# Kernel optimization log

Hardware: AMD Instinct MI355X
Metric: run time of the kernel (lower is better)

The kernel has to match this reference:

```python
import jax, jax.numpy as jnp
import numpy as np

V, D, B, L = 433, 120, 4096, 16  # vocab, d_model, batch, seq_len
H4 = 4 * D
LN_EPS = 1e-5


def setup_inputs() -> dict:
    key = jax.random.key(0)
    ks = jax.random.split(key, 12)
    s = 1.0 / np.sqrt(D)  # PyTorch LSTM init range
    u = lambda k, shape: jax.random.uniform(k, shape, jnp.float32, -s, s)
    return {
        "x": jax.random.randint(ks[0], (B, L), 0, V, dtype=jnp.int32),
        "embed": jax.random.normal(ks[1], (V, D), jnp.float32) * 0.02,
        "Wih0": u(ks[2], (H4, D)), "Whh0": u(ks[3], (H4, D)),
        "bih0": u(ks[4], (H4,)), "bhh0": u(ks[5], (H4,)),
        "Wih1": u(ks[6], (H4, D)), "Whh1": u(ks[7], (H4, D)),
        "bih1": u(ks[8], (H4,)), "bhh1": u(ks[9], (H4,)),
        "gamma": jnp.ones((D,), jnp.float32),
        "beta": jnp.zeros((D,), jnp.float32),
    }


def _lstm_layer(x, Wih, Whh, bih, bhh):
    """One LSTM layer, batch_first input [B,L,D] -> [B,L,H]. PyTorch gate order i,f,g,o."""
    b, _, _ = x.shape
    h_dim = Whh.shape[1]
    # Precompute input contribution for all timesteps in one big GEMM.
    xg = jnp.einsum('bld,gd->blg', x, Wih) + bih + bhh  # [B,L,4H]

    def step(carry, g_t):
        h, c = carry
        gates = g_t + h @ Whh.T  # [B,4H]
        i, f, g, o = jnp.split(gates, 4, axis=-1)
        c = jax.nn.sigmoid(f) * c + jax.nn.sigmoid(i) * jnp.tanh(g)
        h = jax.nn.sigmoid(o) * jnp.tanh(c)
        return (h, c), h

    init = (jnp.zeros((b, h_dim), x.dtype), jnp.zeros((b, h_dim), x.dtype))
    _, hs = jax.lax.scan(step, init, jnp.swapaxes(xg, 0, 1))  # [L,B,H]
    return jnp.swapaxes(hs, 0, 1)


def _layernorm(h, gamma, beta):
    mu = jnp.mean(h, axis=-1, keepdims=True)
    var = jnp.mean(jnp.square(h - mu), axis=-1, keepdims=True)
    return (h - mu) / jnp.sqrt(var + LN_EPS) * gamma + beta


def reference(x, embed, Wih0, Whh0, bih0, bhh0, Wih1, Whh1, bih1, bhh1, gamma, beta):
    h = embed[x]                               # [B,L,D] token embedding
    h = _lstm_layer(h, Wih0, Whh0, bih0, bhh0)  # layer 0
    h = _lstm_layer(h, Wih1, Whh1, bih1, bhh1)  # layer 1
    out = _layernorm(h, gamma, beta)
    logits = jnp.einsum('bld,vd->blv', out, embed)  # tied-embedding head (no bias)
    return logits
```

## Files before the change

kernel.cpp:

```cpp
#include <hip/hip_runtime.h>


#define VSZ 433
#define DIM 120
#define BSZ 4096
#define SEQ 16
#define H4  480
#define MTOT (BSZ*SEQ)
#define KP  128
#define NPAD 448
#define NT_HEAD (NPAD/16)
#define TB  16
#define GP  484
#define HP  136

typedef unsigned int   u32;
typedef unsigned short u16;
typedef __attribute__((ext_vector_type(8))) short    v8bf;
typedef __attribute__((ext_vector_type(8))) _Float16 v8h;
typedef __attribute__((ext_vector_type(4))) float    v4f;

__device__ __forceinline__ float bf2f(u16 u){ union{u32 i;float f;}z; z.i=((u32)u)<<16; return z.f; }
__device__ __forceinline__ u16 f2bf(float f){
  union{float f;u32 u;}z; z.f=f;
  u32 u = z.u + 0x7fffu + ((z.u>>16)&1u);
  return (u16)(u>>16);
}
__device__ __forceinline__ u32 packh2(float a, float b){
  union{_Float16 h[2]; u32 u;} z;
  z.h[0] = (_Float16)a; z.h[1] = (_Float16)b;
  return z.u;
}

#define EW_OFF   0u
#define B1S_OFF  831488u
#define EMBP_OFF 833408u
#define HB0_OFF  948096u

__global__ __launch_bounds__(512) void k_ew(const float* __restrict__ embed,
                                            const float* __restrict__ Wih0,
                                            const float* __restrict__ bih0,
                                            const float* __restrict__ bhh0,
                                            float* __restrict__ EW)
{
  __shared__ float e[DIM];
  const int v = blockIdx.x, tid = threadIdx.x;
  if (tid < DIM) e[tid] = embed[v*DIM + tid];
  __syncthreads();
  if (tid < H4) {
    float acc = bih0[tid] + bhh0[tid];
    #pragma unroll
    for (int k0 = 0; k0 < DIM; k0 += 4) {
      float4 w = *(const float4*)(Wih0 + tid*DIM + k0);
      acc = fmaf(e[k0+0], w.x, acc);
      acc = fmaf(e[k0+1], w.y, acc);
      acc = fmaf(e[k0+2], w.z, acc);
      acc = fmaf(e[k0+3], w.w, acc);
    }
    EW[v*H4 + tid] = acc;
  }
}

__global__ __launch_bounds__(256) void k_prep2(const float* __restrict__ embed,
                                               const float* __restrict__ bih1,
                                               const float* __restrict__ bhh1,
                                               u16* __restrict__ embP,
                                               float* __restrict__ b1s)
{
  const int idx = blockIdx.x*256 + threadIdx.x;
  if (idx < NPAD*KP) {
    int n = idx >> 7, k = idx & 127;
    embP[idx] = (n < VSZ && k < DIM) ? f2bf(embed[n*DIM + k]) : (u16)0;
  } else if (idx < NPAD*KP + H4) {
    int g = idx - NPAD*KP;
    b1s[g] = bih1[g] + bhh1[g];
  }
}

__global__ __launch_bounds__(512) void k_rec0(const float* __restrict__ Whh,
                                              const float* __restrict__ EW,
                                              const int* __restrict__ x,
                                              _Float16* __restrict__ hb0)
{
  __shared__ float gLs[TB][GP];
  __shared__ __align__(16) _Float16 hLh[TB][HP];
  __shared__ int xL[TB*SEQ];

  const int tid  = threadIdx.x;
  const int wave = tid >> 6, lane = tid & 63;
  const int cl   = lane & 15, quad = lane >> 4;
  const int b0   = blockIdx.x * TB;

  for (int i = tid; i < TB*SEQ; i += 512) xL[i] = x[b0*SEQ + i];
  for (int i = tid; i < TB*HP; i += 512) (&hLh[0][0])[i] = (_Float16)0.f;
  __syncthreads();

  v8h Bf[4][4];
  #pragma unroll
  for (int i = 0; i < 4; ++i) {
    const int nt = wave*4 + i;
    const bool vld = (nt < 30);
    const int n = vld ? nt*16 + cl : 0;
    #pragma unroll
    for (int kt = 0; kt < 4; ++kt) {
      const int k0 = kt*32 + quad*8;
      v8h f = {0,0,0,0,0,0,0,0};
      if (vld && k0 < DIM) {
        float4 q0 = *(const float4*)(Whh + n*DIM + k0);
        float4 q1 = *(const float4*)(Whh + n*DIM + k0 + 4);
        f[0]=(_Float16)q0.x; f[1]=(_Float16)q0.y; f[2]=(_Float16)q0.z; f[3]=(_Float16)q0.w;
        f[4]=(_Float16)q1.x; f[5]=(_Float16)q1.y; f[6]=(_Float16)q1.z; f[7]=(_Float16)q1.w;
      }
      Bf[i][kt] = f;
    }
  }

  float srcv[4][4];
  auto load_src = [&](int t) {
    #pragma unroll
    for (int i = 0; i < 4; ++i) {
      const int nt = wave*4 + i;
      if (nt < 30) {
        const int n = nt*16 + cl;
        #pragma unroll
        for (int r = 0; r < 4; ++r)
          srcv[i][r] = EW[(size_t)xL[(quad*4 + r)*SEQ + t]*H4 + n];
      }
    }
  };
  load_src(0);

  const int prow = wave*2;
  const bool act = lane < 60;
  const int d0   = lane*2;
  float C[2][2] = {{0.f,0.f},{0.f,0.f}};

  for (int t = 0; t < SEQ; ++t) {
    __syncthreads();
    v8h Af[4];
    #pragma unroll
    for (int kt = 0; kt < 4; ++kt)
      Af[kt] = *(const v8h*)&hLh[cl][kt*32 + quad*8];
    v4f acc[4];
    #pragma unroll
    for (int i = 0; i < 4; ++i) {
      acc[i][0]=srcv[i][0]; acc[i][1]=srcv[i][1];
      acc[i][2]=srcv[i][2]; acc[i][3]=srcv[i][3];
    }
    #pragma unroll
    for (int i = 0; i < 4; ++i)
      if (wave*4 + i < 30) {
        #pragma unroll
        for (int kt = 0; kt < 4; ++kt)
          acc[i] = __builtin_amdgcn_mfma_f32_16x16x32_f16(Af[kt], Bf[i][kt], acc[i], 0, 0, 0);
      }
    if (t + 1 < SEQ) load_src(t + 1);
    #pragma unroll
    for (int i = 0; i < 4; ++i) {
      const int nt = wave*4 + i;
      if (nt < 30) {
        #pragma unroll
        for (int r = 0; r < 4; ++r)
          gLs[quad*4 + r][nt*16 + cl] = acc[i][r];
      }
    }
    __syncthreads();
    #pragma unroll
    for (int rr = 0; rr < 2; ++rr) {
      const int row = prow + rr;
      if (act) {
        const float2 gi = *(const float2*)&gLs[row][d0      ];
        const float2 gf = *(const float2*)&gLs[row][d0 + 120];
        const float2 gg = *(const float2*)&gLs[row][d0 + 240];
        const float2 go = *(const float2*)&gLs[row][d0 + 360];
        float h2[2];
        #pragma unroll
        for (int k = 0; k < 2; ++k) {
          const float vi = k ? gi.y : gi.x, vf = k ? gf.y : gf.x;
          const float vg = k ? gg.y : gg.x, vo = k ? go.y : go.x;
          const float si = 1.f / (1.f + __expf(-vi));
          const float sf = 1.f / (1.f + __expf(-vf));
          const float tg = 1.f - 2.f / (__expf(2.f*vg) + 1.f);
          const float so = 1.f / (1.f + __expf(-vo));
          const float c  = sf * C[rr][k] + si * tg;
          C[rr][k] = c;
          const float tc = 1.f - 2.f / (__expf(2.f*c) + 1.f);
          h2[k] = so * tc;
        }
        *(u32*)&hLh[row][d0] = packh2(h2[0], h2[1]);
        *(u32*)&hb0[((size_t)t*BSZ + b0 + row)*KP + d0] = packh2(h2[0], h2[1]);
      } else {
        *(u32*)&hb0[((size_t)t*BSZ + b0 + row)*KP + 120 + 2*(lane - 60)] = 0u;
      }
    }
  }
}

__global__ __launch_bounds__(512) void k_rec1(const float* __restrict__ Wih1,
                                              const float* __restrict__ Whh1,
                                              const float* __restrict__ b1s,
                                              const _Float16* __restrict__ hb0,
                                              const float* __restrict__ gamma,
                                              const float* __restrict__ beta,
                                              const u16* __restrict__ embP,
                                              float* __restrict__ out)
{
  __shared__ float gLs[TB][GP];
  __shared__ __align__(16) _Float16 hLh[TB][HP];
  __shared__ __align__(16) u16 hnL[TB][HP];
  __shared__ __align__(16) u16 embL[NPAD][HP];

  const int tid  = threadIdx.x;
  const int wave = tid >> 6, lane = tid & 63;
  const int cl   = lane & 15, quad = lane >> 4;
  const int b0   = blockIdx.x * TB;

  for (int i = tid; i < TB*HP; i += 512) (&hLh[0][0])[i] = (_Float16)0.f;
  for (int c = tid; c < NPAD*16; c += 512) {
    const int rw = c >> 4, c16 = c & 15;
    *(v8bf*)&embL[rw][c16*8] = *(const v8bf*)&embP[(size_t)rw*KP + c16*8];
  }

  v8h Bi[4][4], Bh[4][4];
  float bias[4];
  #pragma unroll
  for (int i = 0; i < 4; ++i) {
    const int nt = wave*4 + i;
    const bool vld = (nt < 30);
    const int n = vld ? nt*16 + cl : 0;
    bias[i] = vld ? b1s[n] : 0.f;
    #pragma unroll
    for (int kt = 0; kt < 4; ++kt) {
      const int k0 = kt*32 + quad*8;
      v8h fi = {0,0,0,0,0,0,0,0}, fh = {0,0,0,0,0,0,0,0};
      if (vld && k0 < DIM) {
        float4 q0 = *(const float4*)(Wih1 + n*DIM + k0);
        float4 q1 = *(const float4*)(Wih1 + n*DIM + k0 + 4);
        fi[0]=(_Float16)q0.x; fi[1]=(_Float16)q0.y; fi[2]=(_Float16)q0.z; fi[3]=(_Float16)q0.w;
        fi[4]=(_Float16)q1.x; fi[5]=(_Float16)q1.y; fi[6]=(_Float16)q1.z; fi[7]=(_Float16)q1.w;
        float4 p0 = *(const float4*)(Whh1 + n*DIM + k0);
        float4 p1 = *(const float4*)(Whh1 + n*DIM + k0 + 4);
        fh[0]=(_Float16)p0.x; fh[1]=(_Float16)p0.y; fh[2]=(_Float16)p0.z; fh[3]=(_Float16)p0.w;
        fh[4]=(_Float16)p1.x; fh[5]=(_Float16)p1.y; fh[6]=(_Float16)p1.z; fh[7]=(_Float16)p1.w;
      }
      Bi[i][kt] = fi;
      Bh[i][kt] = fh;
    }
  }

  const int prow = wave*2;
  const bool act = lane < 60;
  const int d0   = lane*2;
  float gmm[2] = {0.f, 0.f}, bta[2] = {0.f, 0.f};
  if (act) {
    gmm[0] = gamma[d0]; gmm[1] = gamma[d0+1];
    bta[0] = beta[d0];  bta[1] = beta[d0+1];
  }
  float C[2][2] = {{0.f,0.f},{0.f,0.f}};

  v8h A0n[4];
  #pragma unroll
  for (int kt = 0; kt < 4; ++kt)
    A0n[kt] = *(const v8h*)&hb0[((size_t)0*BSZ + b0 + cl)*KP + kt*32 + quad*8];
  __syncthreads();

  for (int t = 0; t < SEQ; ++t) {
    v8h A0c[4], A1[4];
    #pragma unroll
    for (int kt = 0; kt < 4; ++kt) A0c[kt] = A0n[kt];
    #pragma unroll
    for (int kt = 0; kt < 4; ++kt)
      A1[kt] = *(const v8h*)&hLh[cl][kt*32 + quad*8];
    if (t + 1 < SEQ) {
      #pragma unroll
      for (int kt = 0; kt < 4; ++kt)
        A0n[kt] = *(const v8h*)&hb0[((size_t)(t+1)*BSZ + b0 + cl)*KP + kt*32 + quad*8];
    }
    v4f acc[4];
    #pragma unroll
    for (int i = 0; i < 4; ++i)
      acc[i] = (v4f){bias[i], bias[i], bias[i], bias[i]};
    #pragma unroll
    for (int i = 0; i < 4; ++i)
      if (wave*4 + i < 30) {
        #pragma unroll
        for (int kt = 0; kt < 4; ++kt) {
          acc[i] = __builtin_amdgcn_mfma_f32_16x16x32_f16(A0c[kt], Bi[i][kt], acc[i], 0, 0, 0);
          acc[i] = __builtin_amdgcn_mfma_f32_16x16x32_f16(A1[kt],  Bh[i][kt], acc[i], 0, 0, 0);
        }
      }
    #pragma unroll
    for (int i = 0; i < 4; ++i) {
      const int nt = wave*4 + i;
      if (nt < 30) {
        #pragma unroll
        for (int r = 0; r < 4; ++r)
          gLs[quad*4 + r][nt*16 + cl] = acc[i][r];
      }
    }
    __syncthreads();
    float h2[2][2] = {{0.f,0.f},{0.f,0.f}};
    float s1[2] = {0.f, 0.f}, s2[2] = {0.f, 0.f};
    #pragma unroll
    for (int rr = 0; rr < 2; ++rr) {
      const int row = prow + rr;
      if (act) {
        const float2 gi = *(const float2*)&gLs[row][d0      ];
        const float2 gf = *(const float2*)&gLs[row][d0 + 120];
        const float2 gg = *(const float2*)&gLs[row][d0 + 240];
        const float2 go = *(const float2*)&gLs[row][d0 + 360];
        #pragma unroll
        for (int k = 0; k < 2; ++k) {
          const float vi = k ? gi.y : gi.x, vf = k ? gf.y : gf.x;
          const float vg = k ? gg.y : gg.x, vo = k ? go.y : go.x;
          const float si = 1.f / (1.f + __expf(-vi));
          const float sf = 1.f / (1.f + __expf(-vf));
          const float tg = 1.f - 2.f / (__expf(2.f*vg) + 1.f);
          const float so = 1.f / (1.f + __expf(-vo));
          const float c  = sf * C[rr][k] + si * tg;
          C[rr][k] = c;
          const float tc = 1.f - 2.f / (__expf(2.f*c) + 1.f);
          const float h  = so * tc;
          h2[rr][k] = h;
          s1[rr] += h;
          s2[rr] = fmaf(h, h, s2[rr]);
        }
        *(u32*)&hLh[row][d0] = packh2(h2[rr][0], h2[rr][1]);
      }
    }
    #pragma unroll
    for (int m = 32; m >= 1; m >>= 1) {
      s1[0] += __shfl_xor(s1[0], m);
      s2[0] += __shfl_xor(s2[0], m);
      s1[1] += __shfl_xor(s1[1], m);
      s2[1] += __shfl_xor(s2[1], m);
    }
    #pragma unroll
    for (int rr = 0; rr < 2; ++rr) {
      const int row = prow + rr;
      const float mu = s1[rr] * (1.f/DIM);
      const float var = s2[rr] * (1.f/DIM) - mu*mu;
      const float rs = rsqrtf(var + 1e-5f);
      if (act) {
        const float v0 = fmaf((h2[rr][0] - mu)*rs, gmm[0], bta[0]);
        const float v1 = fmaf((h2[rr][1] - mu)*rs, gmm[1], bta[1]);
        *(u32*)&hnL[row][d0] = (u32)f2bf(v0) | ((u32)f2bf(v1) << 16);
      } else {
        *(u32*)&hnL[row][120 + 2*(lane - 60)] = 0u;
      }
    }
    __syncthreads();

    {
      v8bf a[4];
      #pragma unroll
      for (int kt = 0; kt < 4; ++kt)
        a[kt] = *(const v8bf*)&hnL[cl][kt*32 + quad*8];
      #pragma unroll
      for (int j = 0; j < 4; ++j) {
        const int nt = wave + 8*j;
        if (nt < NT_HEAD) {
          const int n = nt*16 + cl;
          v8bf bfr[4];
          #pragma unroll
          for (int kt = 0; kt < 4; ++kt)
            bfr[kt] = *(const v8bf*)&embL[n][kt*32 + quad*8];
          v4f hacc = {0.f, 0.f, 0.f, 0.f};
          #pragma unroll
          for (int kt = 0; kt < 4; ++kt)
            hacc = __builtin_amdgcn_mfma_f32_16x16x32_bf16(a[kt], bfr[kt], hacc, 0, 0, 0);
          if (n < VSZ) {
            #pragma unroll
            for (int r = 0; r < 4; ++r)
              out[((size_t)(b0 + quad*4 + r)*SEQ + t)*VSZ + n] = hacc[r];
          }
        }
      }
    }
  }
}

extern "C" void kernel_launch(void* const* d_in, const int* in_sizes, int n_in,
                              void* d_out, int out_size, void* d_ws, size_t ws_size,
                              hipStream_t stream)
{
  (void)in_sizes; (void)n_in; (void)out_size; (void)ws_size;
  const int*   x     = (const int*)d_in[0];
  const float* embed = (const float*)d_in[1];
  const float* Wih0  = (const float*)d_in[2];
  const float* Whh0  = (const float*)d_in[3];
  const float* bih0  = (const float*)d_in[4];
  const float* bhh0  = (const float*)d_in[5];
  const float* Wih1  = (const float*)d_in[6];
  const float* Whh1  = (const float*)d_in[7];
  const float* bih1  = (const float*)d_in[8];
  const float* bhh1  = (const float*)d_in[9];
  const float* gamma = (const float*)d_in[10];
  const float* beta  = (const float*)d_in[11];

  char* ws = (char*)d_ws;
  float*     EW   = (float*)(ws + EW_OFF);
  float*     b1s  = (float*)(ws + B1S_OFF);
  u16*       embP = (u16*)(ws + EMBP_OFF);
  _Float16*  hb0  = (_Float16*)(ws + HB0_OFF);

  k_ew   <<<VSZ, 512, 0, stream>>>(embed, Wih0, bih0, bhh0, EW);
  k_prep2<<<226, 256, 0, stream>>>(embed, bih1, bhh1, embP, b1s);
  k_rec0 <<<BSZ/TB, 512, 0, stream>>>(Whh0, EW, x, hb0);
  k_rec1 <<<BSZ/TB, 512, 0, stream>>>(Wih1, Whh1, b1s, hb0, gamma, beta, embP, (float*)d_out);
}
```

Measured before the change: 258.3 us.

## Double threads per block in recurrent kernels and read head weights from MFMA-fragment layout

Both recurrent kernels now launch 1024 threads (16 waves) instead of 512, so each wave owns 2 gate tiles and one batch row instead of 4 tiles and two rows. This shortens the serial per-step work on each wave. The layer-1 kernel no longer stages the padded embedding in LDS. Instead it reads bf16 head weights straight from global memory in a fragment-ordered layout built by the prep kernel, and it uses the freed LDS to preload all 16 timesteps of layer-0 output. The trade-offs are more register and occupancy pressure, global or L2 traffic for the head weights on every step, and fewer resident blocks per CU.

```diff
diff --git a/kernel.cpp b/kernel.cpp
--- a/kernel.cpp
+++ b/kernel.cpp
@@ -6,10 +6,9 @@
 #define BSZ 4096
 #define SEQ 16
 #define H4  480
-#define MTOT (BSZ*SEQ)
 #define KP  128
 #define NPAD 448
-#define NT_HEAD (NPAD/16)
+#define NT_HEAD 28
 #define TB  16
 #define GP  484
 #define HP  136
@@ -20,7 +19,6 @@
 typedef __attribute__((ext_vector_type(8))) _Float16 v8h;
 typedef __attribute__((ext_vector_type(4))) float    v4f;
 
-__device__ __forceinline__ float bf2f(u16 u){ union{u32 i;float f;}z; z.i=((u32)u)<<16; return z.f; }
 __device__ __forceinline__ u16 f2bf(float f){
   union{float f;u32 u;}z; z.f=f;
   u32 u = z.u + 0x7fffu + ((z.u>>16)&1u);
@@ -34,7 +32,7 @@
 
 #define EW_OFF   0u
 #define B1S_OFF  831488u
-#define EMBP_OFF 833408u
+#define EMBF_OFF 833408u
 #define HB0_OFF  948096u
 
 __global__ __launch_bounds__(512) void k_ew(const float* __restrict__ embed,
@@ -64,23 +62,25 @@
 __global__ __launch_bounds__(256) void k_prep2(const float* __restrict__ embed,
                                                const float* __restrict__ bih1,
                                                const float* __restrict__ bhh1,
-                                               u16* __restrict__ embP,
+                                               u16* __restrict__ embF,
                                                float* __restrict__ b1s)
 {
   const int idx = blockIdx.x*256 + threadIdx.x;
   if (idx < NPAD*KP) {
     int n = idx >> 7, k = idx & 127;
-    embP[idx] = (n < VSZ && k < DIM) ? f2bf(embed[n*DIM + k]) : (u16)0;
+    int nt = n >> 4, cl = n & 15, kt = k >> 5, quad = (k >> 3) & 3, j = k & 7;
+    int fidx = ((((nt*4 + kt)*4 + quad)*16 + cl) << 3) + j;
+    embF[fidx] = (n < VSZ && k < DIM) ? f2bf(embed[n*DIM + k]) : (u16)0;
   } else if (idx < NPAD*KP + H4) {
     int g = idx - NPAD*KP;
     b1s[g] = bih1[g] + bhh1[g];
   }
 }
 
-__global__ __launch_bounds__(512) void k_rec0(const float* __restrict__ Whh,
-                                              const float* __restrict__ EW,
-                                              const int* __restrict__ x,
-                                              _Float16* __restrict__ hb0)
+__global__ __launch_bounds__(1024) void k_rec0(const float* __restrict__ Whh,
+                                               const float* __restrict__ EW,
+                                               const int* __restrict__ x,
+                                               _Float16* __restrict__ hb0)
 {
   __shared__ float gLs[TB][GP];
   __shared__ __align__(16) _Float16 hLh[TB][HP];
@@ -91,14 +91,15 @@
   const int cl   = lane & 15, quad = lane >> 4;
   const int b0   = blockIdx.x * TB;
 
-  for (int i = tid; i < TB*SEQ; i += 512) xL[i] = x[b0*SEQ + i];
-  for (int i = tid; i < TB*HP; i += 512) (&hLh[0][0])[i] = (_Float16)0.f;
+  for (int i = tid; i < TB*SEQ; i += 1024) xL[i] = x[b0*SEQ + i];
+  for (int i = tid; i < TB*HP; i += 1024) (&hLh[0][0])[i] = (_Float16)0.f;
   __syncthreads();
 
-  v8h Bf[4][4];
+  const int nt0 = wave*2, nt1 = wave*2 + 1;
+  v8h Bf[2][4];
   #pragma unroll
-  for (int i = 0; i < 4; ++i) {
-    const int nt = wave*4 + i;
+  for (int i = 0; i < 2; ++i) {
+    const int nt = wave*2 + i;
     const bool vld = (nt < 30);
     const int n = vld ? nt*16 + cl : 0;
     #pragma unroll
@@ -115,11 +116,11 @@
     }
   }
 
-  float srcv[4][4];
+  float srcv[2][4];
   auto load_src = [&](int t) {
     #pragma unroll
-    for (int i = 0; i < 4; ++i) {
-      const int nt = wave*4 + i;
+    for (int i = 0; i < 2; ++i) {
+      const int nt = wave*2 + i;
       if (nt < 30) {
         const int n = nt*16 + cl;
         #pragma unroll
@@ -130,34 +131,29 @@
   };
   load_src(0);
 
-  const int prow = wave*2;
+  const int row = wave;
   const bool act = lane < 60;
   const int d0   = lane*2;
-  float C[2][2] = {{0.f,0.f},{0.f,0.f}};
+  float C[2] = {0.f, 0.f};
 
   for (int t = 0; t < SEQ; ++t) {
     __syncthreads();
-    v8h Af[4];
-    #pragma unroll
-    for (int kt = 0; kt < 4; ++kt)
-      Af[kt] = *(const v8h*)&hLh[cl][kt*32 + quad*8];
-    v4f acc[4];
-    #pragma unroll
-    for (int i = 0; i < 4; ++i) {
+    v4f acc[2];
+    #pragma unroll
+    for (int i = 0; i < 2; ++i) {
       acc[i][0]=srcv[i][0]; acc[i][1]=srcv[i][1];
       acc[i][2]=srcv[i][2]; acc[i][3]=srcv[i][3];
     }
     #pragma unroll
-    for (int i = 0; i < 4; ++i)
-      if (wave*4 + i < 30) {
-        #pragma unroll
-        for (int kt = 0; kt < 4; ++kt)
-          acc[i] = __builtin_amdgcn_mfma_f32_16x16x32_f16(Af[kt], Bf[i][kt], acc[i], 0, 0, 0);
-      }
+    for (int kt = 0; kt < 4; ++kt) {
+      v8h A1 = *(const v8h*)&hLh[cl][kt*32 + quad*8];
+      if (nt0 < 30) acc[0] = __builtin_amdgcn_mfma_f32_16x16x32_f16(A1, Bf[0][kt], acc[0], 0, 0, 0);
+      if (nt1 < 30) acc[1] = __builtin_amdgcn_mfma_f32_16x16x32_f16(A1, Bf[1][kt], acc[1], 0, 0, 0);
+    }
     if (t + 1 < SEQ) load_src(t + 1);
     #pragma unroll
-    for (int i = 0; i < 4; ++i) {
-      const int nt = wave*4 + i;
+    for (int i = 0; i < 2; ++i) {
+      const int nt = wave*2 + i;
       if (nt < 30) {
         #pragma unroll
         for (int r = 0; r < 4; ++r)
@@ -165,67 +161,64 @@
       }
     }
     __syncthreads();
-    #pragma unroll
-    for (int rr = 0; rr < 2; ++rr) {
-      const int row = prow + rr;
-      if (act) {
-        const float2 gi = *(const float2*)&gLs[row][d0      ];
-        const float2 gf = *(const float2*)&gLs[row][d0 + 120];
-        const float2 gg = *(const float2*)&gLs[row][d0 + 240];
-        const float2 go = *(const float2*)&gLs[row][d0 + 360];
-        float h2[2];
-        #pragma unroll
-        for (int k = 0; k < 2; ++k) {
-          const float vi = k ? gi.y : gi.x, vf = k ? gf.y : gf.x;
-          const float vg = k ? gg.y : gg.x, vo = k ? go.y : go.x;
-          const float si = 1.f / (1.f + __expf(-vi));
-          const float sf = 1.f / (1.f + __expf(-vf));
-          const float tg = 1.f - 2.f / (__expf(2.f*vg) + 1.f);
-          const float so = 1.f / (1.f + __expf(-vo));
-          const float c  = sf * C[rr][k] + si * tg;
-          C[rr][k] = c;
-          const float tc = 1.f - 2.f / (__expf(2.f*c) + 1.f);
-          h2[k] = so * tc;
-        }
-        *(u32*)&hLh[row][d0] = packh2(h2[0], h2[1]);
-        *(u32*)&hb0[((size_t)t*BSZ + b0 + row)*KP + d0] = packh2(h2[0], h2[1]);
-      } else {
-        *(u32*)&hb0[((size_t)t*BSZ + b0 + row)*KP + 120 + 2*(lane - 60)] = 0u;
-      }
-    }
-  }
-}
-
-__global__ __launch_bounds__(512) void k_rec1(const float* __restrict__ Wih1,
-                                              const float* __restrict__ Whh1,
-                                              const float* __restrict__ b1s,
-                                              const _Float16* __restrict__ hb0,
-                                              const float* __restrict__ gamma,
-                                              const float* __restrict__ beta,
-                                              const u16* __restrict__ embP,
-                                              float* __restrict__ out)
+    if (act) {
+      const float2 gi = *(const float2*)&gLs[row][d0      ];
+      const float2 gf = *(const float2*)&gLs[row][d0 + 120];
+      const float2 gg = *(const float2*)&gLs[row][d0 + 240];
+      const float2 go = *(const float2*)&gLs[row][d0 + 360];
+      float h2[2];
+      #pragma unroll
+      for (int k = 0; k < 2; ++k) {
+        const float vi = k ? gi.y : gi.x, vf = k ? gf.y : gf.x;
+        const float vg = k ? gg.y : gg.x, vo = k ? go.y : go.x;
+        const float si = 1.f / (1.f + __expf(-vi));
+        const float sf = 1.f / (1.f + __expf(-vf));
+        const float tg = 1.f - 2.f / (__expf(2.f*vg) + 1.f);
+        const float so = 1.f / (1.f + __expf(-vo));
+        const float c  = sf * C[k] + si * tg;
+        C[k] = c;
+        const float tc = 1.f - 2.f / (__expf(2.f*c) + 1.f);
+        h2[k] = so * tc;
+      }
+      *(u32*)&hLh[row][d0] = packh2(h2[0], h2[1]);
+      *(u32*)&hb0[((size_t)t*BSZ + b0 + row)*KP + d0] = packh2(h2[0], h2[1]);
+    } else {
+      *(u32*)&hb0[((size_t)t*BSZ + b0 + row)*KP + 120 + 2*(lane - 60)] = 0u;
+    }
+  }
+}
+
+__global__ __launch_bounds__(1024) void k_rec1(const float* __restrict__ Wih1,
+                                               const float* __restrict__ Whh1,
+                                               const float* __restrict__ b1s,
+                                               const _Float16* __restrict__ hb0,
+                                               const float* __restrict__ gamma,
+                                               const float* __restrict__ beta,
+                                               const u16* __restrict__ embF,
+                                               float* __restrict__ out)
 {
   __shared__ float gLs[TB][GP];
   __shared__ __align__(16) _Float16 hLh[TB][HP];
   __shared__ __align__(16) u16 hnL[TB][HP];
-  __shared__ __align__(16) u16 embL[NPAD][HP];
+  __shared__ __align__(16) _Float16 hb0L[SEQ][TB][HP];
 
   const int tid  = threadIdx.x;
   const int wave = tid >> 6, lane = tid & 63;
   const int cl   = lane & 15, quad = lane >> 4;
   const int b0   = blockIdx.x * TB;
 
-  for (int i = tid; i < TB*HP; i += 512) (&hLh[0][0])[i] = (_Float16)0.f;
-  for (int c = tid; c < NPAD*16; c += 512) {
-    const int rw = c >> 4, c16 = c & 15;
-    *(v8bf*)&embL[rw][c16*8] = *(const v8bf*)&embP[(size_t)rw*KP + c16*8];
-  }
-
-  v8h Bi[4][4], Bh[4][4];
-  float bias[4];
+  for (int i = tid; i < TB*HP; i += 1024) (&hLh[0][0])[i] = (_Float16)0.f;
+  for (int c = tid; c < SEQ*TB*16; c += 1024) {
+    const int t = c >> 8, rem = c & 255, rw = rem >> 4, k8 = (rem & 15)*8;
+    *(v8h*)&hb0L[t][rw][k8] = *(const v8h*)&hb0[((size_t)t*BSZ + b0 + rw)*KP + k8];
+  }
+
+  const int nt0 = wave*2, nt1 = wave*2 + 1;
+  v8h Bi[2][4], Bh[2][4];
+  float bias[2];
   #pragma unroll
-  for (int i = 0; i < 4; ++i) {
-    const int nt = wave*4 + i;
+  for (int i = 0; i < 2; ++i) {
+    const int nt = wave*2 + i;
     const bool vld = (nt < 30);
     const int n = vld ? nt*16 + cl : 0;
     bias[i] = vld ? b1s[n] : 0.f;
@@ -248,7 +241,7 @@
     }
   }
 
-  const int prow = wave*2;
+  const int row = wave;
   const bool act = lane < 60;
   const int d0   = lane*2;
   float gmm[2] = {0.f, 0.f}, bta[2] = {0.f, 0.f};
@@ -256,42 +249,30 @@
     gmm[0] = gamma[d0]; gmm[1] = gamma[d0+1];
     bta[0] = beta[d0];  bta[1] = beta[d0+1];
   }
-  float C[2][2] = {{0.f,0.f},{0.f,0.f}};
-
-  v8h A0n[4];
-  #pragma unroll
-  for (int kt = 0; kt < 4; ++kt)
-    A0n[kt] = *(const v8h*)&hb0[((size_t)0*BSZ + b0 + cl)*KP + kt*32 + quad*8];
+  float C[2] = {0.f, 0.f};
   __syncthreads();
 
   for (int t = 0; t < SEQ; ++t) {
-    v8h A0c[4], A1[4];
-    #pragma unroll
-    for (int kt = 0; kt < 4; ++kt) A0c[kt] = A0n[kt];
-    #pragma unroll
-    for (int kt = 0; kt < 4; ++kt)
-      A1[kt] = *(const v8h*)&hLh[cl][kt*32 + quad*8];
-    if (t + 1 < SEQ) {
-      #pragma unroll
-      for (int kt = 0; kt < 4; ++kt)
-        A0n[kt] = *(const v8h*)&hb0[((size_t)(t+1)*BSZ + b0 + cl)*KP + kt*32 + quad*8];
-    }
-    v4f acc[4];
-    #pragma unroll
-    for (int i = 0; i < 4; ++i)
+    v4f acc[2];
+    #pragma unroll
+    for (int i = 0; i < 2; ++i)
       acc[i] = (v4f){bias[i], bias[i], bias[i], bias[i]};
     #pragma unroll
-    for (int i = 0; i < 4; ++i)
-      if (wave*4 + i < 30) {
-        #pragma unroll
-        for (int kt = 0; kt < 4; ++kt) {
-          acc[i] = __builtin_amdgcn_mfma_f32_16x16x32_f16(A0c[kt], Bi[i][kt], acc[i], 0, 0, 0);
-          acc[i] = __builtin_amdgcn_mfma_f32_16x16x32_f16(A1[kt],  Bh[i][kt], acc[i], 0, 0, 0);
-        }
-      }
-    #pragma unroll
-    for (int i = 0; i < 4; ++i) {
-      const int nt = wave*4 + i;
+    for (int kt = 0; kt < 4; ++kt) {
+      v8h A0 = *(const v8h*)&hb0L[t][cl][kt*32 + quad*8];
+      v8h A1 = *(const v8h*)&hLh[cl][kt*32 + quad*8];
+      if (nt0 < 30) {
+        acc[0] = __builtin_amdgcn_mfma_f32_16x16x32_f16(A0, Bi[0][kt], acc[0], 0, 0, 0);
+        acc[0] = __builtin_amdgcn_mfma_f32_16x16x32_f16(A1, Bh[0][kt], acc[0], 0, 0, 0);
+      }
+      if (nt1 < 30) {
+        acc[1] = __builtin_amdgcn_mfma_f32_16x16x32_f16(A0, Bi[1][kt], acc[1], 0, 0, 0);
+        acc[1] = __builtin_amdgcn_mfma_f32_16x16x32_f16(A1, Bh[1][kt], acc[1], 0, 0, 0);
+      }
+    }
+    #pragma unroll
+    for (int i = 0; i < 2; ++i) {
+      const int nt = wave*2 + i;
       if (nt < 30) {
         #pragma unroll
         for (int r = 0; r < 4; ++r)
@@ -299,51 +280,43 @@
       }
     }
     __syncthreads();
-    float h2[2][2] = {{0.f,0.f},{0.f,0.f}};
-    float s1[2] = {0.f, 0.f}, s2[2] = {0.f, 0.f};
-    #pragma unroll
-    for (int rr = 0; rr < 2; ++rr) {
-      const int row = prow + rr;
-      if (act) {
-        const float2 gi = *(const float2*)&gLs[row][d0      ];
-        const float2 gf = *(const float2*)&gLs[row][d0 + 120];
-        const float2 gg = *(const float2*)&gLs[row][d0 + 240];
-        const float2 go = *(const float2*)&gLs[row][d0 + 360];
-        #pragma unroll
-        for (int k = 0; k < 2; ++k) {
-          const float vi = k ? gi.y : gi.x, vf = k ? gf.y : gf.x;
-          const float vg = k ? gg.y : gg.x, vo = k ? go.y : go.x;
-          const float si = 1.f / (1.f + __expf(-vi));
-          const float sf = 1.f / (1.f + __expf(-vf));
-          const float tg = 1.f - 2.f / (__expf(2.f*vg) + 1.f);
-          const float so = 1.f / (1.f + __expf(-vo));
-          const float c  = sf * C[rr][k] + si * tg;
-          C[rr][k] = c;
-          const float tc = 1.f - 2.f / (__expf(2.f*c) + 1.f);
-          const float h  = so * tc;
-          h2[rr][k] = h;
-          s1[rr] += h;
-          s2[rr] = fmaf(h, h, s2[rr]);
-        }
-        *(u32*)&hLh[row][d0] = packh2(h2[rr][0], h2[rr][1]);
-      }
+    float h2[2] = {0.f, 0.f};
+    float s1 = 0.f, s2 = 0.f;
+    if (act) {
+      const float2 gi = *(const float2*)&gLs[row][d0      ];
+      const float2 gf = *(const float2*)&gLs[row][d0 + 120];
+      const float2 gg = *(const float2*)&gLs[row][d0 + 240];
+      const float2 go = *(const float2*)&gLs[row][d0 + 360];
+      #pragma unroll
+      for (int k = 0; k < 2; ++k) {
+        const float vi = k ? gi.y : gi.x, vf = k ? gf.y : gf.x;
+        const float vg = k ? gg.y : gg.x, vo = k ? go.y : go.x;
+        const float si = 1.f / (1.f + __expf(-vi));
+        const float sf = 1.f / (1.f + __expf(-vf));
+        const float tg = 1.f - 2.f / (__expf(2.f*vg) + 1.f);
+        const float so = 1.f / (1.f + __expf(-vo));
+        const float c  = sf * C[k] + si * tg;
+        C[k] = c;
+        const float tc = 1.f - 2.f / (__expf(2.f*c) + 1.f);
+        const float h  = so * tc;
+        h2[k] = h;
+        s1 += h;
+        s2 = fmaf(h, h, s2);
+      }
+      *(u32*)&hLh[row][d0] = packh2(h2[0], h2[1]);
     }
     #pragma unroll
     for (int m = 32; m >= 1; m >>= 1) {
-      s1[0] += __shfl_xor(s1[0], m);
-      s2[0] += __shfl_xor(s2[0], m);
-      s1[1] += __shfl_xor(s1[1], m);
-      s2[1] += __shfl_xor(s2[1], m);
-    }
-    #pragma unroll
-    for (int rr = 0; rr < 2; ++rr) {
-      const int row = prow + rr;
-      const float mu = s1[rr] * (1.f/DIM);
-      const float var = s2[rr] * (1.f/DIM) - mu*mu;
+      s1 += __shfl_xor(s1, m);
+      s2 += __shfl_xor(s2, m);
+    }
+    {
+      const float mu = s1 * (1.f/DIM);
+      const float var = s2 * (1.f/DIM) - mu*mu;
       const float rs = rsqrtf(var + 1e-5f);
       if (act) {
-        const float v0 = fmaf((h2[rr][0] - mu)*rs, gmm[0], bta[0]);
-        const float v1 = fmaf((h2[rr][1] - mu)*rs, gmm[1], bta[1]);
+        const float v0 = fmaf((h2[0] - mu)*rs, gmm[0], bta[0]);
+        const float v1 = fmaf((h2[1] - mu)*rs, gmm[1], bta[1]);
         *(u32*)&hnL[row][d0] = (u32)f2bf(v0) | ((u32)f2bf(v1) << 16);
       } else {
         *(u32*)&hnL[row][120 + 2*(lane - 60)] = 0u;
@@ -357,18 +330,18 @@
       for (int kt = 0; kt < 4; ++kt)
         a[kt] = *(const v8bf*)&hnL[cl][kt*32 + quad*8];
       #pragma unroll
-      for (int j = 0; j < 4; ++j) {
-        const int nt = wave + 8*j;
+      for (int j = 0; j < 2; ++j) {
+        const int nt = wave + 16*j;
         if (nt < NT_HEAD) {
-          const int n = nt*16 + cl;
           v8bf bfr[4];
           #pragma unroll
           for (int kt = 0; kt < 4; ++kt)
-            bfr[kt] = *(const v8bf*)&embL[n][kt*32 + quad*8];
+            bfr[kt] = *(const v8bf*)&embF[(((size_t)nt*4 + kt)*64 + lane)*8];
           v4f hacc = {0.f, 0.f, 0.f, 0.f};
           #pragma unroll
           for (int kt = 0; kt < 4; ++kt)
             hacc = __builtin_amdgcn_mfma_f32_16x16x32_bf16(a[kt], bfr[kt], hacc, 0, 0, 0);
+          const int n = nt*16 + cl;
           if (n < VSZ) {
             #pragma unroll
             for (int r = 0; r < 4; ++r)
@@ -401,11 +374,11 @@
   char* ws = (char*)d_ws;
   float*     EW   = (float*)(ws + EW_OFF);
   float*     b1s  = (float*)(ws + B1S_OFF);
-  u16*       embP = (u16*)(ws + EMBP_OFF);
+  u16*       embF = (u16*)(ws + EMBF_OFF);
   _Float16*  hb0  = (_Float16*)(ws + HB0_OFF);
 
   k_ew   <<<VSZ, 512, 0, stream>>>(embed, Wih0, bih0, bhh0, EW);
-  k_prep2<<<226, 256, 0, stream>>>(embed, bih1, bhh1, embP, b1s);
-  k_rec0 <<<BSZ/TB, 512, 0, stream>>>(Whh0, EW, x, hb0);
-  k_rec1 <<<BSZ/TB, 512, 0, stream>>>(Wih1, Whh1, b1s, hb0, gamma, beta, embP, (float*)d_out);
-}
+  k_prep2<<<226, 256, 0, stream>>>(embed, bih1, bhh1, embF, b1s);
+  k_rec0 <<<BSZ/TB, 1024, 0, stream>>>(Whh0, EW, x, hb0);
+  k_rec1 <<<BSZ/TB, 1024, 0, stream>>>(Wih1, Whh1, b1s, hb0, gamma, beta, embF, (float*)d_out);
+}
```

After: 287.8 us. 1.11x slower.

## Fuse both LSTM layers and head into one wavefront-pipelined recurrent kernel

Applied to the files above, without the earlier changes.

Merges the layer-0 and layer-1 recurrent kernels into a single kernel that runs layer 0 at step s, layer 1 at step s-1 and the tied-embedding head at step s-2 in the same loop iteration. This removes the global round trip of the layer-0 hidden states and one of the two per-step barrier chains. Wih1 and the embedding are pre-swizzled into MFMA fragment order in global memory and read directly, rather than kept in registers or staged in a large LDS copy. The cost is extra per-step global loads of the Wih1 and embedding fragments, plus higher register pressure from holding both layers' state.

```diff
diff --git a/kernel.cpp b/kernel.cpp
--- a/kernel.cpp
+++ b/kernel.cpp
@@ -6,10 +6,9 @@
 #define BSZ 4096
 #define SEQ 16
 #define H4  480
-#define MTOT (BSZ*SEQ)
 #define KP  128
 #define NPAD 448
-#define NT_HEAD (NPAD/16)
+#define NT_HEAD 28
 #define TB  16
 #define GP  484
 #define HP  136
@@ -20,7 +19,6 @@
 typedef __attribute__((ext_vector_type(8))) _Float16 v8h;
 typedef __attribute__((ext_vector_type(4))) float    v4f;
 
-__device__ __forceinline__ float bf2f(u16 u){ union{u32 i;float f;}z; z.i=((u32)u)<<16; return z.f; }
 __device__ __forceinline__ u16 f2bf(float f){
   union{float f;u32 u;}z; z.f=f;
   u32 u = z.u + 0x7fffu + ((z.u>>16)&1u);
@@ -34,8 +32,8 @@
 
 #define EW_OFF   0u
 #define B1S_OFF  831488u
-#define EMBP_OFF 833408u
-#define HB0_OFF  948096u
+#define EMBF_OFF 833408u
+#define W1F_OFF  948096u
 
 __global__ __launch_bounds__(512) void k_ew(const float* __restrict__ embed,
                                             const float* __restrict__ Wih0,
@@ -61,29 +59,48 @@
   }
 }
 
-__global__ __launch_bounds__(256) void k_prep2(const float* __restrict__ embed,
-                                               const float* __restrict__ bih1,
-                                               const float* __restrict__ bhh1,
-                                               u16* __restrict__ embP,
-                                               float* __restrict__ b1s)
+__global__ __launch_bounds__(256) void k_prep(const float* __restrict__ embed,
+                                              const float* __restrict__ bih1,
+                                              const float* __restrict__ bhh1,
+                                              const float* __restrict__ Wih1,
+                                              u16* __restrict__ embF,
+                                              float* __restrict__ b1s,
+                                              _Float16* __restrict__ w1F)
 {
   const int idx = blockIdx.x*256 + threadIdx.x;
   if (idx < NPAD*KP) {
     int n = idx >> 7, k = idx & 127;
-    embP[idx] = (n < VSZ && k < DIM) ? f2bf(embed[n*DIM + k]) : (u16)0;
+    int nt = n >> 4, cl = n & 15, kt = k >> 5, quad = (k >> 3) & 3, j = k & 7;
+    int fidx = ((((nt*4 + kt)*4 + quad)*16 + cl) << 3) + j;
+    embF[fidx] = (n < VSZ && k < DIM) ? f2bf(embed[n*DIM + k]) : (u16)0;
   } else if (idx < NPAD*KP + H4) {
     int g = idx - NPAD*KP;
     b1s[g] = bih1[g] + bhh1[g];
-  }
-}
-
-__global__ __launch_bounds__(512) void k_rec0(const float* __restrict__ Whh,
-                                              const float* __restrict__ EW,
-                                              const int* __restrict__ x,
-                                              _Float16* __restrict__ hb0)
+  } else if (idx < NPAD*KP + H4 + 30*4*512) {
+    int i0 = idx - (NPAD*KP + H4);
+    int f = i0 >> 9, r = i0 & 511, lane = r >> 3, j = r & 7;
+    int nt = f >> 2, kt = f & 3, cl = lane & 15, quad = lane >> 4;
+    int k = kt*32 + quad*8 + j, n = nt*16 + cl;
+    w1F[i0] = (k < DIM) ? (_Float16)Wih1[n*DIM + k] : (_Float16)0.f;
+  }
+}
+
+__global__ __launch_bounds__(512) void k_rec(const float* __restrict__ Whh0,
+                                             const float* __restrict__ EW,
+                                             const int* __restrict__ x,
+                                             const float* __restrict__ Whh1,
+                                             const float* __restrict__ b1s,
+                                             const float* __restrict__ gamma,
+                                             const float* __restrict__ beta,
+                                             const _Float16* __restrict__ w1F,
+                                             const u16* __restrict__ embF,
+                                             float* __restrict__ out)
 {
-  __shared__ float gLs[TB][GP];
-  __shared__ __align__(16) _Float16 hLh[TB][HP];
+  __shared__ float gLs0[TB][GP];
+  __shared__ float gLs1[TB][GP];
+  __shared__ __align__(16) _Float16 hLh0[TB][HP];
+  __shared__ __align__(16) _Float16 hLh1[TB][HP];
+  __shared__ __align__(16) u16 hnLD[2][TB][HP];
   __shared__ int xL[TB*SEQ];
 
   const int tid  = threadIdx.x;
@@ -92,26 +109,35 @@
   const int b0   = blockIdx.x * TB;
 
   for (int i = tid; i < TB*SEQ; i += 512) xL[i] = x[b0*SEQ + i];
-  for (int i = tid; i < TB*HP; i += 512) (&hLh[0][0])[i] = (_Float16)0.f;
-  __syncthreads();
-
-  v8h Bf[4][4];
+  for (int i = tid; i < TB*HP; i += 512) {
+    (&hLh0[0][0])[i] = (_Float16)0.f;
+    (&hLh1[0][0])[i] = (_Float16)0.f;
+  }
+
+  v8h Bf0[4][4], Bh1[4][4];
+  float bias[4];
   #pragma unroll
   for (int i = 0; i < 4; ++i) {
     const int nt = wave*4 + i;
     const bool vld = (nt < 30);
     const int n = vld ? nt*16 + cl : 0;
+    bias[i] = vld ? b1s[n] : 0.f;
     #pragma unroll
     for (int kt = 0; kt < 4; ++kt) {
       const int k0 = kt*32 + quad*8;
-      v8h f = {0,0,0,0,0,0,0,0};
+      v8h f0 = {0,0,0,0,0,0,0,0}, f1 = {0,0,0,0,0,0,0,0};
       if (vld && k0 < DIM) {
-        float4 q0 = *(const float4*)(Whh + n*DIM + k0);
-        float4 q1 = *(const float4*)(Whh + n*DIM + k0 + 4);
-        f[0]=(_Float16)q0.x; f[1]=(_Float16)q0.y; f[2]=(_Float16)q0.z; f[3]=(_Float16)q0.w;
-        f[4]=(_Float16)q1.x; f[5]=(_Float16)q1.y; f[6]=(_Float16)q1.z; f[7]=(_Float16)q1.w;
-      }
-      Bf[i][kt] = f;
+        float4 q0 = *(const float4*)(Whh0 + n*DIM + k0);
+        float4 q1 = *(const float4*)(Whh0 + n*DIM + k0 + 4);
+        f0[0]=(_Float16)q0.x; f0[1]=(_Float16)q0.y; f0[2]=(_Float16)q0.z; f0[3]=(_Float16)q0.w;
+        f0[4]=(_Float16)q1.x; f0[5]=(_Float16)q1.y; f0[6]=(_Float16)q1.z; f0[7]=(_Float16)q1.w;
+        float4 p0 = *(const float4*)(Whh1 + n*DIM + k0);
+        float4 p1 = *(const float4*)(Whh1 + n*DIM + k0 + 4);
+        f1[0]=(_Float16)p0.x; f1[1]=(_Float16)p0.y; f1[2]=(_Float16)p0.z; f1[3]=(_Float16)p0.w;
+        f1[4]=(_Float16)p1.x; f1[5]=(_Float16)p1.y; f1[6]=(_Float16)p1.z; f1[7]=(_Float16)p1.w;
+      }
+      Bf0[i][kt] = f0;
+      Bh1[i][kt] = f1;
     }
   }
 
@@ -133,247 +159,187 @@
   const int prow = wave*2;
   const bool act = lane < 60;
   const int d0   = lane*2;
-  float C[2][2] = {{0.f,0.f},{0.f,0.f}};
-
-  for (int t = 0; t < SEQ; ++t) {
-    __syncthreads();
-    v8h Af[4];
-    #pragma unroll
-    for (int kt = 0; kt < 4; ++kt)
-      Af[kt] = *(const v8h*)&hLh[cl][kt*32 + quad*8];
-    v4f acc[4];
-    #pragma unroll
-    for (int i = 0; i < 4; ++i) {
-      acc[i][0]=srcv[i][0]; acc[i][1]=srcv[i][1];
-      acc[i][2]=srcv[i][2]; acc[i][3]=srcv[i][3];
-    }
-    #pragma unroll
-    for (int i = 0; i < 4; ++i)
-      if (wave*4 + i < 30) {
-        #pragma unroll
-        for (int kt = 0; kt < 4; ++kt)
-          acc[i] = __builtin_amdgcn_mfma_f32_16x16x32_f16(Af[kt], Bf[i][kt], acc[i], 0, 0, 0);
-      }
-    if (t + 1 < SEQ) load_src(t + 1);
-    #pragma unroll
-    for (int i = 0; i < 4; ++i) {
-      const int nt = wave*4 + i;
-      if (nt < 30) {
-        #pragma unroll
-        for (int r = 0; r < 4; ++r)
-          gLs[quad*4 + r][nt*16 + cl] = acc[i][r];
-      }
-    }
-    __syncthreads();
-    #pragma unroll
-    for (int rr = 0; rr < 2; ++rr) {
-      const int row = prow + rr;
-      if (act) {
-        const float2 gi = *(const float2*)&gLs[row][d0      ];
-        const float2 gf = *(const float2*)&gLs[row][d0 + 120];
-        const float2 gg = *(const float2*)&gLs[row][d0 + 240];
-        const float2 go = *(const float2*)&gLs[row][d0 + 360];
-        float h2[2];
-        #pragma unroll
-        for (int k = 0; k < 2; ++k) {
-          const float vi = k ? gi.y : gi.x, vf = k ? gf.y : gf.x;
-          const float vg = k ? gg.y : gg.x, vo = k ? go.y : go.x;
-          const float si = 1.f / (1.f + __expf(-vi));
-          const float sf = 1.f / (1.f + __expf(-vf));
-          const float tg = 1.f - 2.f / (__expf(2.f*vg) + 1.f);
-          const float so = 1.f / (1.f + __expf(-vo));
-          const float c  = sf * C[rr][k] + si * tg;
-          C[rr][k] = c;
-          const float tc = 1.f - 2.f / (__expf(2.f*c) + 1.f);
-          h2[k] = so * tc;
-        }
-        *(u32*)&hLh[row][d0] = packh2(h2[0], h2[1]);
-        *(u32*)&hb0[((size_t)t*BSZ + b0 + row)*KP + d0] = packh2(h2[0], h2[1]);
-      } else {
-        *(u32*)&hb0[((size_t)t*BSZ + b0 + row)*KP + 120 + 2*(lane - 60)] = 0u;
-      }
-    }
-  }
-}
-
-__global__ __launch_bounds__(512) void k_rec1(const float* __restrict__ Wih1,
-                                              const float* __restrict__ Whh1,
-                                              const float* __restrict__ b1s,
-                                              const _Float16* __restrict__ hb0,
-                                              const float* __restrict__ gamma,
-                                              const float* __restrict__ beta,
-                                              const u16* __restrict__ embP,
-                                              float* __restrict__ out)
-{
-  __shared__ float gLs[TB][GP];
-  __shared__ __align__(16) _Float16 hLh[TB][HP];
-  __shared__ __align__(16) u16 hnL[TB][HP];
-  __shared__ __align__(16) u16 embL[NPAD][HP];
-
-  const int tid  = threadIdx.x;
-  const int wave = tid >> 6, lane = tid & 63;
-  const int cl   = lane & 15, quad = lane >> 4;
-  const int b0   = blockIdx.x * TB;
-
-  for (int i = tid; i < TB*HP; i += 512) (&hLh[0][0])[i] = (_Float16)0.f;
-  for (int c = tid; c < NPAD*16; c += 512) {
-    const int rw = c >> 4, c16 = c & 15;
-    *(v8bf*)&embL[rw][c16*8] = *(const v8bf*)&embP[(size_t)rw*KP + c16*8];
-  }
-
-  v8h Bi[4][4], Bh[4][4];
-  float bias[4];
-  #pragma unroll
-  for (int i = 0; i < 4; ++i) {
-    const int nt = wave*4 + i;
-    const bool vld = (nt < 30);
-    const int n = vld ? nt*16 + cl : 0;
-    bias[i] = vld ? b1s[n] : 0.f;
-    #pragma unroll
-    for (int kt = 0; kt < 4; ++kt) {
-      const int k0 = kt*32 + quad*8;
-      v8h fi = {0,0,0,0,0,0,0,0}, fh = {0,0,0,0,0,0,0,0};
-      if (vld && k0 < DIM) {
-        float4 q0 = *(const float4*)(Wih1 + n*DIM + k0);
-        float4 q1 = *(const float4*)(Wih1 + n*DIM + k0 + 4);
-        fi[0]=(_Float16)q0.x; fi[1]=(_Float16)q0.y; fi[2]=(_Float16)q0.z; fi[3]=(_Float16)q0.w;
-        fi[4]=(_Float16)q1.x; fi[5]=(_Float16)q1.y; fi[6]=(_Float16)q1.z; fi[7]=(_Float16)q1.w;
-        float4 p0 = *(const float4*)(Whh1 + n*DIM + k0);
-        float4 p1 = *(const float4*)(Whh1 + n*DIM + k0 + 4);
-        fh[0]=(_Float16)p0.x; fh[1]=(_Float16)p0.y; fh[2]=(_Float16)p0.z; fh[3]=(_Float16)p0.w;
-        fh[4]=(_Float16)p1.x; fh[5]=(_Float16)p1.y; fh[6]=(_Float16)p1.z; fh[7]=(_Float16)p1.w;
-      }
-      Bi[i][kt] = fi;
-      Bh[i][kt] = fh;
-    }
-  }
-
-  const int prow = wave*2;
-  const bool act = lane < 60;
-  const int d0   = lane*2;
   float gmm[2] = {0.f, 0.f}, bta[2] = {0.f, 0.f};
   if (act) {
     gmm[0] = gamma[d0]; gmm[1] = gamma[d0+1];
     bta[0] = beta[d0];  bta[1] = beta[d0+1];
   }
-  float C[2][2] = {{0.f,0.f},{0.f,0.f}};
-
-  v8h A0n[4];
-  #pragma unroll
-  for (int kt = 0; kt < 4; ++kt)
-    A0n[kt] = *(const v8h*)&hb0[((size_t)0*BSZ + b0 + cl)*KP + kt*32 + quad*8];
+  float C0[2][2] = {{0.f,0.f},{0.f,0.f}};
+  float C1[2][2] = {{0.f,0.f},{0.f,0.f}};
   __syncthreads();
 
-  for (int t = 0; t < SEQ; ++t) {
-    v8h A0c[4], A1[4];
-    #pragma unroll
-    for (int kt = 0; kt < 4; ++kt) A0c[kt] = A0n[kt];
-    #pragma unroll
-    for (int kt = 0; kt < 4; ++kt)
-      A1[kt] = *(const v8h*)&hLh[cl][kt*32 + quad*8];
-    if (t + 1 < SEQ) {
+  for (int s = 0; s <= SEQ; ++s) {
+    v4f acc0[4], acc1[4];
+    #pragma unroll
+    for (int i = 0; i < 4; ++i) {
+      acc0[i][0]=srcv[i][0]; acc0[i][1]=srcv[i][1];
+      acc0[i][2]=srcv[i][2]; acc0[i][3]=srcv[i][3];
+      acc1[i] = (v4f){bias[i], bias[i], bias[i], bias[i]};
+    }
+    #pragma unroll
+    for (int kt = 0; kt < 4; ++kt) {
+      v8h hbF = *(const v8h*)&hLh0[cl][kt*32 + quad*8];
+      v8h h1F = *(const v8h*)&hLh1[cl][kt*32 + quad*8];
+      #pragma unroll
+      for (int i = 0; i < 4; ++i) {
+        const int nt = wave*4 + i;
+        if (nt < 30) {
+          if (s < SEQ)
+            acc0[i] = __builtin_amdgcn_mfma_f32_16x16x32_f16(hbF, Bf0[i][kt], acc0[i], 0, 0, 0);
+          if (s >= 1) {
+            v8h w1f = *(const v8h*)&w1F[(((size_t)nt*4 + kt)*64 + lane)*8];
+            acc1[i] = __builtin_amdgcn_mfma_f32_16x16x32_f16(hbF, w1f, acc1[i], 0, 0, 0);
+            acc1[i] = __builtin_amdgcn_mfma_f32_16x16x32_f16(h1F, Bh1[i][kt], acc1[i], 0, 0, 0);
+          }
+        }
+      }
+    }
+    if (s >= 2) {
+      const int t = s - 2;
+      v8bf a[4];
       #pragma unroll
       for (int kt = 0; kt < 4; ++kt)
-        A0n[kt] = *(const v8h*)&hb0[((size_t)(t+1)*BSZ + b0 + cl)*KP + kt*32 + quad*8];
-    }
-    v4f acc[4];
-    #pragma unroll
-    for (int i = 0; i < 4; ++i)
-      acc[i] = (v4f){bias[i], bias[i], bias[i], bias[i]};
-    #pragma unroll
-    for (int i = 0; i < 4; ++i)
-      if (wave*4 + i < 30) {
-        #pragma unroll
-        for (int kt = 0; kt < 4; ++kt) {
-          acc[i] = __builtin_amdgcn_mfma_f32_16x16x32_f16(A0c[kt], Bi[i][kt], acc[i], 0, 0, 0);
-          acc[i] = __builtin_amdgcn_mfma_f32_16x16x32_f16(A1[kt],  Bh[i][kt], acc[i], 0, 0, 0);
-        }
-      }
-    #pragma unroll
-    for (int i = 0; i < 4; ++i) {
-      const int nt = wave*4 + i;
-      if (nt < 30) {
-        #pragma unroll
-        for (int r = 0; r < 4; ++r)
-          gLs[quad*4 + r][nt*16 + cl] = acc[i][r];
-      }
-    }
-    __syncthreads();
-    float h2[2][2] = {{0.f,0.f},{0.f,0.f}};
-    float s1[2] = {0.f, 0.f}, s2[2] = {0.f, 0.f};
-    #pragma unroll
-    for (int rr = 0; rr < 2; ++rr) {
-      const int row = prow + rr;
-      if (act) {
-        const float2 gi = *(const float2*)&gLs[row][d0      ];
-        const float2 gf = *(const float2*)&gLs[row][d0 + 120];
-        const float2 gg = *(const float2*)&gLs[row][d0 + 240];
-        const float2 go = *(const float2*)&gLs[row][d0 + 360];
-        #pragma unroll
-        for (int k = 0; k < 2; ++k) {
-          const float vi = k ? gi.y : gi.x, vf = k ? gf.y : gf.x;
-          const float vg = k ? gg.y : gg.x, vo = k ? go.y : go.x;
-          const float si = 1.f / (1.f + __expf(-vi));
-          const float sf = 1.f / (1.f + __expf(-vf));
-          const float tg = 1.f - 2.f / (__expf(2.f*vg) + 1.f);
-          const float so = 1.f / (1.f + __expf(-vo));
-          const float c  = sf * C[rr][k] + si * tg;
-          C[rr][k] = c;
-          const float tc = 1.f - 2.f / (__expf(2.f*c) + 1.f);
-          const float h  = so * tc;
-          h2[rr][k] = h;
-          s1[rr] += h;
-          s2[rr] = fmaf(h, h, s2[rr]);
-        }
-        *(u32*)&hLh[row][d0] = packh2(h2[rr][0], h2[rr][1]);
-      }
-    }
-    #pragma unroll
-    for (int m = 32; m >= 1; m >>= 1) {
-      s1[0] += __shfl_xor(s1[0], m);
-      s2[0] += __shfl_xor(s2[0], m);
-      s1[1] += __shfl_xor(s1[1], m);
-      s2[1] += __shfl_xor(s2[1], m);
-    }
-    #pragma unroll
-    for (int rr = 0; rr < 2; ++rr) {
-      const int row = prow + rr;
-      const float mu = s1[rr] * (1.f/DIM);
-      const float var = s2[rr] * (1.f/DIM) - mu*mu;
-      const float rs = rsqrtf(var + 1e-5f);
-      if (act) {
-        const float v0 = fmaf((h2[rr][0] - mu)*rs, gmm[0], bta[0]);
-        const float v1 = fmaf((h2[rr][1] - mu)*rs, gmm[1], bta[1]);
-        *(u32*)&hnL[row][d0] = (u32)f2bf(v0) | ((u32)f2bf(v1) << 16);
-      } else {
-        *(u32*)&hnL[row][120 + 2*(lane - 60)] = 0u;
-      }
-    }
-    __syncthreads();
-
-    {
-      v8bf a[4];
-      #pragma unroll
-      for (int kt = 0; kt < 4; ++kt)
-        a[kt] = *(const v8bf*)&hnL[cl][kt*32 + quad*8];
+        a[kt] = *(const v8bf*)&hnLD[s & 1][cl][kt*32 + quad*8];
       #pragma unroll
       for (int j = 0; j < 4; ++j) {
-        const int nt = wave + 8*j;
-        if (nt < NT_HEAD) {
-          const int n = nt*16 + cl;
+        const int nth = wave + 8*j;
+        if (nth < NT_HEAD) {
           v8bf bfr[4];
           #pragma unroll
           for (int kt = 0; kt < 4; ++kt)
-            bfr[kt] = *(const v8bf*)&embL[n][kt*32 + quad*8];
+            bfr[kt] = *(const v8bf*)&embF[(((size_t)nth*4 + kt)*64 + lane)*8];
           v4f hacc = {0.f, 0.f, 0.f, 0.f};
           #pragma unroll
           for (int kt = 0; kt < 4; ++kt)
             hacc = __builtin_amdgcn_mfma_f32_16x16x32_bf16(a[kt], bfr[kt], hacc, 0, 0, 0);
+          const int n = nth*16 + cl;
           if (n < VSZ) {
             #pragma unroll
             for (int r = 0; r < 4; ++r)
               out[((size_t)(b0 + quad*4 + r)*SEQ + t)*VSZ + n] = hacc[r];
           }
+        }
+      }
+    }
+    if (s + 1 < SEQ) load_src(s + 1);
+    #pragma unroll
+    for (int i = 0; i < 4; ++i) {
+      const int nt = wave*4 + i;
+      if (nt < 30) {
+        #pragma unroll
+        for (int r = 0; r < 4; ++r) {
+          if (s < SEQ) gLs0[quad*4 + r][nt*16 + cl] = acc0[i][r];
+          if (s >= 1) gLs1[quad*4 + r][nt*16 + cl] = acc1[i][r];
+        }
+      }
+    }
+    __syncthreads();
+
+    if (s < SEQ) {
+      #pragma unroll
+      for (int rr = 0; rr < 2; ++rr) {
+        const int row = prow + rr;
+        if (act) {
+          const float2 gi = *(const float2*)&gLs0[row][d0      ];
+          const float2 gf = *(const float2*)&gLs0[row][d0 + 120];
+          const float2 gg = *(const float2*)&gLs0[row][d0 + 240];
+          const float2 go = *(const float2*)&gLs0[row][d0 + 360];
+          float h2[2];
+          #pragma unroll
+          for (int k = 0; k < 2; ++k) {
+            const float vi = k ? gi.y : gi.x, vf = k ? gf.y : gf.x;
+            const float vg = k ? gg.y : gg.x, vo = k ? go.y : go.x;
+            const float si = 1.f / (1.f + __expf(-vi));
+            const float sf = 1.f / (1.f + __expf(-vf));
+            const float tg = 1.f - 2.f / (__expf(2.f*vg) + 1.f);
+            const float so = 1.f / (1.f + __expf(-vo));
+            const float c  = sf * C0[rr][k] + si * tg;
+            C0[rr][k] = c;
+            const float tc = 1.f - 2.f / (__expf(2.f*c) + 1.f);
+            h2[k] = so * tc;
+          }
+          *(u32*)&hLh0[row][d0] = packh2(h2[0], h2[1]);
+        }
+      }
+    }
+    if (s >= 1) {
+      float h2[2][2] = {{0.f,0.f},{0.f,0.f}};
+      float s1[2] = {0.f, 0.f}, s2[2] = {0.f, 0.f};
+      #pragma unroll
+      for (int rr = 0; rr < 2; ++rr) {
+        const int row = prow + rr;
+        if (act) {
+          const float2 gi = *(const float2*)&gLs1[row][d0      ];
+          const float2 gf = *(const float2*)&gLs1[row][d0 + 120];
+          const float2 gg = *(const float2*)&gLs1[row][d0 + 240];
+          const float2 go = *(const float2*)&gLs1[row][d0 + 360];
+          #pragma unroll
+          for (int k = 0; k < 2; ++k) {
+            const float vi = k ? gi.y : gi.x, vf = k ? gf.y : gf.x;
+            const float vg = k ? gg.y : gg.x, vo = k ? go.y : go.x;
+            const float si = 1.f / (1.f + __expf(-vi));
+            const float sf = 1.f / (1.f + __expf(-vf));
+            const float tg = 1.f - 2.f / (__expf(2.f*vg) + 1.f);
+            const float so = 1.f / (1.f + __expf(-vo));
+            const float c  = sf * C1[rr][k] + si * tg;
+            C1[rr][k] = c;
+            const float tc = 1.f - 2.f / (__expf(2.f*c) + 1.f);
+            const float h  = so * tc;
+            h2[rr][k] = h;
+            s1[rr] += h;
+            s2[rr] = fmaf(h, h, s2[rr]);
+          }
+          *(u32*)&hLh1[row][d0] = packh2(h2[rr][0], h2[rr][1]);
+        }
+      }
+      #pragma unroll
+      for (int m = 32; m >= 1; m >>= 1) {
+        s1[0] += __shfl_xor(s1[0], m);
+        s2[0] += __shfl_xor(s2[0], m);
+        s1[1] += __shfl_xor(s1[1], m);
+        s2[1] += __shfl_xor(s2[1], m);
+      }
+      #pragma unroll
+      for (int rr = 0; rr < 2; ++rr) {
+        const int row = prow + rr;
+        const float mu = s1[rr] * (1.f/DIM);
+        const float var = s2[rr] * (1.f/DIM) - mu*mu;
+        const float rs = rsqrtf(var + 1e-5f);
+        if (act) {
+          const float v0 = fmaf((h2[rr][0] - mu)*rs, gmm[0], bta[0]);
+          const float v1 = fmaf((h2[rr][1] - mu)*rs, gmm[1], bta[1]);
+          *(u32*)&hnLD[(s-1) & 1][row][d0] = (u32)f2bf(v0) | ((u32)f2bf(v1) << 16);
+        } else {
+          *(u32*)&hnLD[(s-1) & 1][row][120 + 2*(lane - 60)] = 0u;
+        }
+      }
+    }
+    __syncthreads();
+  }
+
+  {
+    const int t = SEQ - 1;
+    v8bf a[4];
+    #pragma unroll
+    for (int kt = 0; kt < 4; ++kt)
+      a[kt] = *(const v8bf*)&hnLD[1][cl][kt*32 + quad*8];
+    #pragma unroll
+    for (int j = 0; j < 4; ++j) {
+      const int nth = wave + 8*j;
+      if (nth < NT_HEAD) {
+        v8bf bfr[4];
+        #pragma unroll
+        for (int kt = 0; kt < 4; ++kt)
+          bfr[kt] = *(const v8bf*)&embF[(((size_t)nth*4 + kt)*64 + lane)*8];
+        v4f hacc = {0.f, 0.f, 0.f, 0.f};
+        #pragma unroll
+        for (int kt = 0; kt < 4; ++kt)
+          hacc = __builtin_amdgcn_mfma_f32_16x16x32_bf16(a[kt], bfr[kt], hacc, 0, 0, 0);
+        const int n = nth*16 + cl;
+        if (n < VSZ) {
+          #pragma unroll
+          for (int r = 0; r < 4; ++r)
+            out[((size_t)(b0 + quad*4 + r)*SEQ + t)*VSZ + n] = hacc[r];
         }
       }
     }
@@ -401,11 +367,10 @@
   char* ws = (char*)d_ws;
   float*     EW   = (float*)(ws + EW_OFF);
   float*     b1s  = (float*)(ws + B1S_OFF);
-  u16*       embP = (u16*)(ws + EMBP_OFF);
-  _Float16*  hb0  = (_Float16*)(ws + HB0_OFF);
-
-  k_ew   <<<VSZ, 512, 0, stream>>>(embed, Wih0, bih0, bhh0, EW);
-  k_prep2<<<226, 256, 0, stream>>>(embed, bih1, bhh1, embP, b1s);
-  k_rec0 <<<BSZ/TB, 512, 0, stream>>>(Whh0, EW, x, hb0);
-  k_rec1 <<<BSZ/TB, 512, 0, stream>>>(Wih1, Whh1, b1s, hb0, gamma, beta, embP, (float*)d_out);
-}
+  u16*       embF = (u16*)(ws + EMBF_OFF);
+  _Float16*  w1F  = (_Float16*)(ws + W1F_OFF);
+
+  k_ew  <<<VSZ, 512, 0, stream>>>(embed, Wih0, bih0, bhh0, EW);
+  k_prep<<<466, 256, 0, stream>>>(embed, bih1, bhh1, Wih1, embF, b1s, w1F);
+  k_rec <<<BSZ/TB, 512, 0, stream>>>(Whh0, EW, x, Whh1, b1s, gamma, beta, w1F, embF, (float*)d_out);
+}
```

Result: slower. 548.1 us (+112.2%).
